# Optimization experiments

Hardware: AMD Instinct MI355X
Metric: run time of the kernel (lower is better)

Reference implementation:

```python
import jax, jax.numpy as jnp
import numpy as np

WS = 7          # window size
NH = 12         # attention heads
D_STATE = 64    # mamba d_state
HEADDIM = 64    # mamba headdim


def layernorm(x, w, b):
    mu = jnp.mean(x, axis=-1, keepdims=True)
    var = jnp.mean((x - mu) ** 2, axis=-1, keepdims=True)
    return (x - mu) * jax.lax.rsqrt(var + 1e-5) * w + b


def mamba2(x, W_in, conv_w, conv_b, dt_bias, A_log, D, mnorm_w, W_out):
    # Mamba2 (SSD) forward: in_proj -> causal depthwise conv+silu -> selective scan -> gated RMSNorm -> out_proj
    B, L, dm = x.shape
    nheads = dt_bias.shape[0]
    d_inner = nheads * HEADDIM
    zxbcdt = x @ W_in                                   # (B,L,2*d_inner+2*d_state+nheads)
    z = zxbcdt[..., :d_inner]
    xBC = zxbcdt[..., d_inner:2 * d_inner + 2 * D_STATE]
    dt = zxbcdt[..., -nheads:]
    conv_dim = xBC.shape[-1]
    pad = conv_w.shape[-1] - 1
    xBC_t = jnp.swapaxes(xBC, 1, 2)                     # (B, conv_dim, L)
    conv_out = jax.lax.conv_general_dilated(
        xBC_t, conv_w[:, None, :], window_strides=(1,), padding=[(pad, 0)],
        feature_group_count=conv_dim, dimension_numbers=('NCH', 'OIH', 'NCH'))
    xBC = jax.nn.silu(jnp.swapaxes(conv_out, 1, 2) + conv_b)
    xs = xBC[..., :d_inner]
    Bm = xBC[..., d_inner:d_inner + D_STATE]            # (B,L,n)
    Cm = xBC[..., d_inner + D_STATE:]                   # (B,L,n)
    dt = jax.nn.softplus(dt + dt_bias)                  # (B,L,h)
    A = -jnp.exp(A_log)                                 # (h,)
    dA = jnp.exp(dt * A)                                # (B,L,h)
    xh = xs.reshape(B, L, nheads, HEADDIM)              # (B,L,h,p)

    def step(h, inp):
        dA_t, dt_t, x_t, B_t, C_t = inp                 # (B,h),(B,h),(B,h,p),(B,n),(B,n)
        dBx = (dt_t[..., None] * x_t)[..., None] * B_t[:, None, None, :]
        h = h * dA_t[..., None, None] + dBx             # (B,h,p,n)
        y = jnp.einsum('bhpn,bn->bhp', h, C_t)
        return h, y

    sw = lambda a: jnp.swapaxes(a, 0, 1)                # time-major
    h0 = jnp.zeros((B, nheads, HEADDIM, D_STATE), x.dtype)
    _, ys = jax.lax.scan(step, h0, (sw(dA), sw(dt), sw(xh), sw(Bm), sw(Cm)))
    y = jnp.swapaxes(ys, 0, 1) + D[None, None, :, None] * xh   # (B,L,h,p)
    y = y.reshape(B, L, d_inner)
    g = y * jax.nn.silu(z)                              # gated RMSNorm (norm_before_gate=False)
    g = g * jax.lax.rsqrt(jnp.mean(g * g, axis=-1, keepdims=True) + 1e-5) * mnorm_w
    return g @ W_out


def gated_window_attention(xw, qkv_w, qkv_b, gate_w, gate_b, proj_w, proj_b):
    B_, N, C = xw.shape
    hd = C // NH
    qkv = (xw @ qkv_w + qkv_b).reshape(B_, N, 3, NH, hd).transpose(2, 0, 3, 1, 4)
    q, k, v = qkv[0] * (hd ** -0.5), qkv[1], qkv[2]     # (B_,h,N,d)
    attn = jax.nn.softmax(jnp.einsum('bhnd,bhmd->bhnm', q, k), axis=-1)
    xa = jnp.einsum('bhnm,bhmd->bhnd', attn, v).transpose(0, 2, 1, 3)  # (B_,N,h,d)
    gate = jax.nn.sigmoid(xw @ gate_w + gate_b)[..., None]             # (B_,N,h,1)
    xa = (xa * gate).reshape(B_, N, C)
    return xa @ proj_w + proj_b


def lgs_forward(x, norm1_w, norm1_b, W_in, conv_w, conv_b, dt_bias, A_log, D, mnorm_w, W_out,
                qkv_w, qkv_b, gate_w, gate_b, proj_w, proj_b, fusion_w, fusion_b,
                norm2_w, norm2_b, fc1_w, fc1_b, fc2_w, fc2_b, H, W):
    B, L, C = x.shape
    shortcut = x
    xn = layernorm(x, norm1_w, norm1_b)
    # Branch A: Mamba2 global scan
    x_mamba = mamba2(xn, W_in, conv_w, conv_b, dt_bias, A_log, D, mnorm_w, W_out)
    # Branch B: gated window attention (shift_size=0 -> no roll, no mask)
    x2d = xn.reshape(B, H, W, C)
    xw = x2d.reshape(B, H // WS, WS, W // WS, WS, C).transpose(0, 1, 3, 2, 4, 5).reshape(-1, WS * WS, C)
    aw = gated_window_attention(xw, qkv_w, qkv_b, gate_w, gate_b, proj_w, proj_b)
    x_attn = aw.reshape(B, H // WS, W // WS, WS, WS, C).transpose(0, 1, 3, 2, 4, 5).reshape(B, L, C)
    # Fuse branches with 1x1 conv (== linear on channel dim)
    x_cat = jnp.concatenate([x_mamba, x_attn], axis=-1)   # (B,L,2C)
    x_fused = x_cat @ fusion_w + fusion_b
    x = shortcut + x_fused
    xn2 = layernorm(x, norm2_w, norm2_b)
    mlp = jax.nn.gelu(xn2 @ fc1_w + fc1_b, approximate=False) @ fc2_w + fc2_b
    return x + mlp


def setup_inputs() -> dict:
    key = jax.random.key(0)
    ks = jax.random.split(key, 16)
    B, H, W, C = 8, 56, 56, 384
    L = H * W
    d_inner, d_state, nheads_m, d_conv = 768, 64, 12, 4
    d_in_proj = 2 * d_inner + 2 * d_state + nheads_m   # 1676
    conv_dim = d_inner + 2 * d_state                   # 896
    s = 0.02
    return {
        'x': jax.random.normal(ks[0], (B, L, C), jnp.float32),
        'norm1_w': jnp.ones((C,), jnp.float32),
        'norm1_b': jnp.zeros((C,), jnp.float32),
        'W_in': jax.random.normal(ks[1], (C, d_in_proj), jnp.float32) * s,
        'conv_w': jax.random.normal(ks[2], (conv_dim, d_conv), jnp.float32) * 0.1,
        'conv_b': jnp.zeros((conv_dim,), jnp.float32),
        'dt_bias': jax.random.normal(ks[3], (nheads_m,), jnp.float32) * 0.5,
        'A_log': jnp.log(jax.random.uniform(ks[4], (nheads_m,), jnp.float32, 1.0, 16.0)),
        'D': jnp.ones((nheads_m,), jnp.float32),
        'mnorm_w': jnp.ones((d_inner,), jnp.float32),
        'W_out': jax.random.normal(ks[5], (d_inner, C), jnp.float32) * s,
        'qkv_w': jax.random.normal(ks[6], (C, 3 * C), jnp.float32) * s,
        'qkv_b': jnp.zeros((3 * C,), jnp.float32),
        'gate_w': jax.random.normal(ks[7], (C, NH), jnp.float32) * s,
        'gate_b': jnp.zeros((NH,), jnp.float32),
        'proj_w': jax.random.normal(ks[8], (C, C), jnp.float32) * s,
        'proj_b': jnp.zeros((C,), jnp.float32),
        'fusion_w': jax.random.normal(ks[9], (2 * C, C), jnp.float32) * s,
        'fusion_b': jnp.zeros((C,), jnp.float32),
        'norm2_w': jnp.ones((C,), jnp.float32),
        'norm2_b': jnp.zeros((C,), jnp.float32),
        'fc1_w': jax.random.normal(ks[10], (C, 4 * C), jnp.float32) * s,
        'fc1_b': jnp.zeros((4 * C,), jnp.float32),
        'fc2_w': jax.random.normal(ks[11], (4 * C, C), jnp.float32) * s,
        'fc2_b': jnp.zeros((C,), jnp.float32),
        'H': H,
        'W': W,
    }


def reference(x, norm1_w, norm1_b, W_in, conv_w, conv_b, dt_bias, A_log, D, mnorm_w, W_out,
              qkv_w, qkv_b, gate_w, gate_b, proj_w, proj_b, fusion_w, fusion_b,
              norm2_w, norm2_b, fc1_w, fc1_b, fc2_w, fc2_b, H, W):
    return lgs_forward(x, norm1_w, norm1_b, W_in, conv_w, conv_b, dt_bias, A_log, D, mnorm_w, W_out,
                       qkv_w, qkv_b, gate_w, gate_b, proj_w, proj_b, fusion_w, fusion_b,
                       norm2_w, norm2_b, fc1_w, fc1_b, fc2_w, fc2_b, H, W)
```

## Files before the change

### kernel.cpp

```cpp
#include <hip/hip_runtime.h>
#include <math.h>

static constexpr int L_SEQ  = 3136;
static constexpr int NBATCH = 8;
static constexpr int CDIM   = 384;
static constexpr int DIN    = 768;
static constexpr int NHM    = 12;
static constexpr int HDM    = 64;
static constexpr int DPROJ  = 1676;
static constexpr int CONVD  = 896;
static constexpr int NROWS  = NBATCH * L_SEQ;
static constexpr int NHA    = 12;
static constexpr int NCH    = 49;
static constexpr int CHT    = 64;
static constexpr int CTK    = 28;

typedef __attribute__((ext_vector_type(8))) short short8;
typedef __attribute__((ext_vector_type(8))) unsigned short ushort8;
typedef __attribute__((ext_vector_type(4))) float f32x4;
typedef const unsigned int __attribute__((address_space(1)))* gua_t;
typedef unsigned int __attribute__((address_space(3)))* lua_t;

__device__ __forceinline__ float siluf(float x) { return x / (1.f + __expf(-x)); }
__device__ __forceinline__ unsigned short f2bf(float f) {
  unsigned int u = __float_as_uint(f);
  u += 0x7fff + ((u >> 16) & 1);
  return (unsigned short)(u >> 16);
}
__device__ __forceinline__ float bf2f(unsigned short h) {
  return __uint_as_float(((unsigned int)h) << 16);
}

__global__ __launch_bounds__(256) void ln_kernel(const float* __restrict__ in,
    const float* __restrict__ w, const float* __restrict__ b, unsigned short* __restrict__ out) {
  int wave = threadIdx.x >> 6, lane = threadIdx.x & 63;
  int row = blockIdx.x * 4 + wave;
  if (row >= NROWS) return;
  const float* r = in + (size_t)row * CDIM;
  float2 v[3];
  float s1 = 0.f, s2 = 0.f;
#pragma unroll
  for (int q = 0; q < 3; q++) {
    v[q] = *(const float2*)&r[q * 128 + lane * 2];
    s1 += v[q].x + v[q].y;
    s2 += v[q].x * v[q].x + v[q].y * v[q].y;
  }
#pragma unroll
  for (int o = 32; o > 0; o >>= 1) { s1 += __shfl_xor(s1, o, 64); s2 += __shfl_xor(s2, o, 64); }
  float mu = s1 * (1.f / 384.f);
  float var = s2 * (1.f / 384.f) - mu * mu;
  float rs = rsqrtf(var + 1e-5f);
  unsigned short* o = out + (size_t)row * CDIM;
#pragma unroll
  for (int q = 0; q < 3; q++) {
    int c = q * 128 + lane * 2;
    float2 wv = *(const float2*)&w[c];
    float2 bv = *(const float2*)&b[c];
    float ox = (v[q].x - mu) * rs * wv.x + bv.x;
    float oy = (v[q].y - mu) * rs * wv.y + bv.y;
    unsigned int pk = (unsigned int)f2bf(ox) | ((unsigned int)f2bf(oy) << 16);
    *(unsigned int*)&o[c] = pk;
  }
}

__global__ __launch_bounds__(256) void wconv_kernel(const float* __restrict__ W,
    unsigned short* __restrict__ WT, int K, int N, int ldw) {
  __shared__ float tile[32][33];
  int k0 = blockIdx.x * 32, n0 = blockIdx.y * 32;
  int tx = threadIdx.x & 31, ty = threadIdx.x >> 5;
#pragma unroll
  for (int j = 0; j < 4; j++) {
    int k = k0 + ty + j * 8;
    int n = n0 + tx;
    tile[ty + j * 8][tx] = (n < N) ? W[(size_t)k * ldw + n] : 0.f;
  }
  __syncthreads();
#pragma unroll
  for (int j = 0; j < 4; j++) {
    int n = n0 + ty + j * 8;
    int k = k0 + tx;
    WT[(size_t)n * K + k] = f2bf(tile[tx][ty + j * 8]);
  }
}

template<int ACT, bool HASBIAS, bool HASRES, bool OUTBF>
__global__ __launch_bounds__(256) void gemm_bf(
    const unsigned short* __restrict__ A, const unsigned short* __restrict__ WT,
    void* __restrict__ Cp, const float* __restrict__ bias,
    const float* __restrict__ res, int ldr,
    int M, int N, int K, int lda, int ldc, int coff)
{
  __shared__ unsigned short As[128][32];
  __shared__ unsigned short Ws[128][32];
  int t = threadIdx.x;
  int m0 = blockIdx.y * 128, n0 = blockIdx.x * 128;
  int lane = t & 63, w = t >> 6;
  int wr = (w >> 1) * 64, wc = (w & 1) * 64;
  int fl = lane & 15, kq = lane >> 4;
  f32x4 acc[4][4];
#pragma unroll
  for (int i = 0; i < 4; i++)
#pragma unroll
    for (int j = 0; j < 4; j++) acc[i][j] = (f32x4)0.f;

  for (int k0 = 0; k0 < K; k0 += 32) {
#pragma unroll
    for (int j = 0; j < 2; j++) {
      int c = j * 256 + t;
      int row = c >> 2, q = c & 3;
      __builtin_amdgcn_global_load_lds(
          (gua_t)&A[(size_t)(m0 + row) * lda + k0 + q * 8],
          (lua_t)&As[0][0] + (size_t)c * 4, 16, 0, 0);
      __builtin_amdgcn_global_load_lds(
          (gua_t)&WT[(size_t)(n0 + row) * K + k0 + q * 8],
          (lua_t)&Ws[0][0] + (size_t)c * 4, 16, 0, 0);
    }
    __syncthreads();
    short8 af[4], bfr[4];
#pragma unroll
    for (int mi = 0; mi < 4; mi++) af[mi] = *(const short8*)&As[wr + mi * 16 + fl][kq * 8];
#pragma unroll
    for (int ni = 0; ni < 4; ni++) bfr[ni] = *(const short8*)&Ws[wc + ni * 16 + fl][kq * 8];
#pragma unroll
    for (int mi = 0; mi < 4; mi++)
#pragma unroll
      for (int ni = 0; ni < 4; ni++)
        acc[mi][ni] = __builtin_amdgcn_mfma_f32_16x16x32_bf16(af[mi], bfr[ni], acc[mi][ni], 0, 0, 0);
    __syncthreads();
  }
  int rbase = (lane >> 4) * 4, cl = lane & 15;
#pragma unroll
  for (int mi = 0; mi < 4; mi++) {
#pragma unroll
    for (int ni = 0; ni < 4; ni++) {
      int n = n0 + wc + ni * 16 + cl;
      if (n >= N) continue;
#pragma unroll
      for (int r = 0; r < 4; r++) {
        int m = m0 + wr + mi * 16 + rbase + r;
        float v = acc[mi][ni][r];
        if (HASBIAS) v += bias[n];
        if (ACT == 1) v = 0.5f * v * (1.f + erff(v * 0.70710678118654752f));
        if (HASRES) v += res[(size_t)m * ldr + n];
        if (OUTBF) ((unsigned short*)Cp)[(size_t)m * ldc + coff + n] = f2bf(v);
        else       ((float*)Cp)[(size_t)m * ldc + coff + n] = v;
      }
    }
  }
}

__global__ void dtprep_kernel(float* __restrict__ DT, const float* __restrict__ dt_bias,
    const float* __restrict__ A_log, float* __restrict__ DA) {
  int idx = blockIdx.x * blockDim.x + threadIdx.x;
  if (idx >= NROWS * NHM) return;
  int h = idx % NHM;
  float v = DT[idx] + dt_bias[h];
  float sp = (v > 20.f) ? v : log1pf(expf(v));
  DT[idx] = sp;
  DA[idx] = -expf(A_log[h]) * sp;
}

__global__ __launch_bounds__(256) void conv_bf_kernel(const unsigned short* __restrict__ xbc,
    const float* __restrict__ cw, const float* __restrict__ cb, unsigned short* __restrict__ XC) {
  int t = blockIdx.x * 256 + threadIdx.x;
  int c8 = t % 112;
  int rg = t / 112;
  int b = rg / 112, lc = rg % 112;
  int l0 = lc * CTK;
  int c0 = c8 * 8;
  float w0[8], w1[8], w2[8], w3[8], bq[8];
#pragma unroll
  for (int i = 0; i < 8; i++) {
    bq[i] = cb[c0 + i];
    float4 w4 = *(const float4*)&cw[(c0 + i) * 4];
    w0[i] = w4.x; w1[i] = w4.y; w2[i] = w4.z; w3[i] = w4.w;
  }
  const unsigned short* base = xbc + (size_t)b * L_SEQ * CONVD + c0;
  unsigned short* obase = XC + (size_t)b * L_SEQ * CONVD + c0;
  ushort8 h0 = (ushort8)0, h1 = (ushort8)0, h2 = (ushort8)0;
  if (l0 >= 3) {
    h0 = *(const ushort8*)&base[(size_t)(l0 - 3) * CONVD];
    h1 = *(const ushort8*)&base[(size_t)(l0 - 2) * CONVD];
    h2 = *(const ushort8*)&base[(size_t)(l0 - 1) * CONVD];
  }
  for (int i = 0; i < CTK; i++) {
    ushort8 cur = *(const ushort8*)&base[(size_t)(l0 + i) * CONVD];
    ushort8 ov;
#pragma unroll
    for (int q = 0; q < 8; q++) {
      float acc = bq[q] + w0[q] * bf2f(h0[q]) + w1[q] * bf2f(h1[q])
                + w2[q] * bf2f(h2[q]) + w3[q] * bf2f(cur[q]);
      ov[q] = f2bf(siluf(acc));
    }
    *(ushort8*)&obase[(size_t)(l0 + i) * CONVD] = ov;
    h0 = h1; h1 = h2; h2 = cur;
  }
}

__global__ __launch_bounds__(256) void mscan1_kernel(const unsigned short* __restrict__ XC,
    const float* __restrict__ dtp, const float* __restrict__ dta,
    float* __restrict__ H, float* __restrict__ QS) {
  __shared__ unsigned short Xt[64 * 72];
  __shared__ unsigned short Bt[64 * 72];
  __shared__ float lcs[64];
  __shared__ float wss[64];
  int ch = blockIdx.x, bh = blockIdx.y;
  int b = bh / NHM, head = bh - b * NHM;
  int t = threadIdx.x;
  int l0 = ch * CHT;
  const unsigned short* xcb = XC + ((size_t)b * L_SEQ + l0) * CONVD;
  if (t < 64) {
    size_t ro = ((size_t)b * L_SEQ + l0 + t) * NHM + head;
    float s = dta[ro];
#pragma unroll
    for (int o = 1; o < 64; o <<= 1) {
      float u = __shfl_up(s, o, 64);
      if (t >= o) s += u;
    }
    float lc63 = __shfl(s, 63, 64);
    lcs[t] = s;
    wss[t] = dtp[ro] * __expf(lc63 - s);
    if (t == 63) QS[bh * NCH + ch] = __expf(s);
  }
  __syncthreads();
#pragma unroll
  for (int it = 0; it < 16; it++) {
    int e = it * 256 + t;
    int j = e >> 6, cc = e & 63;
    const unsigned short* rowp = xcb + (size_t)j * CONVD;
    Xt[cc * 72 + j] = rowp[head * HDM + cc];
    Bt[cc * 72 + j] = f2bf(bf2f(rowp[768 + cc]) * wss[j]);
  }
  __syncthreads();
  int lane = t & 63, w = t >> 6;
  int wr = (w >> 1) * 32, wc = (w & 1) * 32;
  int fl = lane & 15, kq = lane >> 4;
  f32x4 acc[2][2];
#pragma unroll
  for (int i = 0; i < 2; i++)
#pragma unroll
    for (int j = 0; j < 2; j++) acc[i][j] = (f32x4)0.f;
#pragma unroll
  for (int kk = 0; kk < 2; kk++) {
    short8 af[2], bfr[2];
#pragma unroll
    for (int mi = 0; mi < 2; mi++)
      af[mi] = *(const short8*)&Xt[(wr + mi * 16 + fl) * 72 + kk * 32 + kq * 8];
#pragma unroll
    for (int ni = 0; ni < 2; ni++)
      bfr[ni] = *(const short8*)&Bt[(wc + ni * 16 + fl) * 72 + kk * 32 + kq * 8];
#pragma unroll
    for (int mi = 0; mi < 2; mi++)
#pragma unroll
      for (int ni = 0; ni < 2; ni++)
        acc[mi][ni] = __builtin_amdgcn_mfma_f32_16x16x32_bf16(af[mi], bfr[ni], acc[mi][ni], 0, 0, 0);
  }
  float* Hp = H + ((size_t)bh * NCH + ch) * 4096;
  int rbase = kq * 4, cl = fl;
#pragma unroll
  for (int mi = 0; mi < 2; mi++)
#pragma unroll
    for (int ni = 0; ni < 2; ni++)
#pragma unroll
      for (int r = 0; r < 4; r++)
        Hp[(size_t)(wr + mi * 16 + rbase + r) * 64 + wc + ni * 16 + cl] = acc[mi][ni][r];
}

__global__ __launch_bounds__(64) void scomb_kernel(float* __restrict__ H,
    const float* __restrict__ QS) {
  int bh = blockIdx.x;
  int e = (blockIdx.y * 64 + threadIdx.x) * 4;
  float4 cur = make_float4(0.f, 0.f, 0.f, 0.f);
  for (int s = 0; s < NCH; s++) {
    float* Hp = H + ((size_t)bh * NCH + s) * 4096 + e;
    float q = QS[bh * NCH + s];
    float4 tmp = *(float4*)Hp;
    *(float4*)Hp = cur;
    cur.x = q * cur.x + tmp.x;
    cur.y = q * cur.y + tmp.y;
    cur.z = q * cur.z + tmp.z;
    cur.w = q * cur.w + tmp.w;
  }
}

__global__ __launch_bounds__(256) void mscan2_kernel(const unsigned short* __restrict__ XC,
    const float* __restrict__ dtp, const float* __restrict__ dta,
    const float* __restrict__ H, const float* __restrict__ Dp,
    unsigned short* __restrict__ Ybf) {
  __shared__ unsigned short Cs[64 * 72];
  __shared__ unsigned short Bs[64 * 72];
  __shared__ unsigned short Xt[64 * 72];
  __shared__ unsigned short Hs[64 * 72];
  __shared__ unsigned short Ss[64 * 72];
  __shared__ float lcs[64];
  __shared__ float dts[64];
  int ch = blockIdx.x, bh = blockIdx.y;
  int b = bh / NHM, head = bh - b * NHM;
  int t = threadIdx.x;
  int l0 = ch * CHT;
  const unsigned short* xcb = XC + ((size_t)b * L_SEQ + l0) * CONVD;
  const float* Hg = H + ((size_t)bh * NCH + ch) * 4096;
  if (t < 64) {
    size_t ro = ((size_t)b * L_SEQ + l0 + t) * NHM + head;
    float s = dta[ro];
#pragma unroll
    for (int o = 1; o < 64; o <<= 1) {
      float u = __shfl_up(s, o, 64);
      if (t >= o) s += u;
    }
    lcs[t] = s;
    dts[t] = dtp[ro];
  }
#pragma unroll
  for (int it = 0; it < 16; it++) {
    int e = it * 256 + t;
    int j = e >> 6, cc = e & 63;
    const unsigned short* rowp = xcb + (size_t)j * CONVD;
    Xt[cc * 72 + j] = rowp[head * HDM + cc];
    Bs[j * 72 + cc] = rowp[768 + cc];
    Cs[j * 72 + cc] = rowp[832 + cc];
    Hs[j * 72 + cc] = f2bf(Hg[e]);
  }
  __syncthreads();
  int lane = t & 63, w = t >> 6;
  int wr = (w >> 1) * 32, wc = (w & 1) * 32;
  int fl = lane & 15, kq = lane >> 4;
  int rbase = kq * 4, cl = fl;
  f32x4 sacc[2][2];
#pragma unroll
  for (int i = 0; i < 2; i++)
#pragma unroll
    for (int j = 0; j < 2; j++) sacc[i][j] = (f32x4)0.f;
#pragma unroll
  for (int kk = 0; kk < 2; kk++) {
    short8 af[2], bfr[2];
#pragma unroll
    for (int mi = 0; mi < 2; mi++)
      af[mi] = *(const short8*)&Cs[(wr + mi * 16 + fl) * 72 + kk * 32 + kq * 8];
#pragma unroll
    for (int ni = 0; ni < 2; ni++)
      bfr[ni] = *(const short8*)&Bs[(wc + ni * 16 + fl) * 72 + kk * 32 + kq * 8];
#pragma unroll
    for (int mi = 0; mi < 2; mi++)
#pragma unroll
      for (int ni = 0; ni < 2; ni++)
        sacc[mi][ni] = __builtin_amdgcn_mfma_f32_16x16x32_bf16(af[mi], bfr[ni], sacc[mi][ni], 0, 0, 0);
  }
  __syncthreads();
#pragma unroll
  for (int mi = 0; mi < 2; mi++)
#pragma unroll
    for (int ni = 0; ni < 2; ni++)
#pragma unroll
      for (int r = 0; r < 4; r++) {
        int i = wr + mi * 16 + rbase + r;
        int j = wc + ni * 16 + cl;
        float v = (j <= i) ? sacc[mi][ni][r] * dts[j] * __expf(lcs[i] - lcs[j]) : 0.f;
        Ss[i * 72 + j] = f2bf(v);
      }
#pragma unroll
  for (int it = 0; it < 16; it++) {
    int e = it * 256 + t;
    int i = e >> 6, n = e & 63;
    float cv = bf2f(Cs[i * 72 + n]) * __expf(lcs[i]);
    Cs[i * 72 + n] = f2bf(cv);
  }
  __syncthreads();
  f32x4 yacc[2][2];
#pragma unroll
  for (int i = 0; i < 2; i++)
#pragma unroll
    for (int j = 0; j < 2; j++) yacc[i][j] = (f32x4)0.f;
#pragma unroll
  for (int kk = 0; kk < 2; kk++) {
    short8 af[2], bfr[2];
#pragma unroll
    for (int mi = 0; mi < 2; mi++)
      af[mi] = *(const short8*)&Ss[(wr + mi * 16 + fl) * 72 + kk * 32 + kq * 8];
#pragma unroll
    for (int ni = 0; ni < 2; ni++)
      bfr[ni] = *(const short8*)&Xt[(wc + ni * 16 + fl) * 72 + kk * 32 + kq * 8];
#pragma unroll
    for (int mi = 0; mi < 2; mi++)
#pragma unroll
      for (int ni = 0; ni < 2; ni++)
        yacc[mi][ni] = __builtin_amdgcn_mfma_f32_16x16x32_bf16(af[mi], bfr[ni], yacc[mi][ni], 0, 0, 0);
  }
#pragma unroll
  for (int kk = 0; kk < 2; kk++) {
    short8 af[2], bfr[2];
#pragma unroll
    for (int mi = 0; mi < 2; mi++)
      af[mi] = *(const short8*)&Cs[(wr + mi * 16 + fl) * 72 + kk * 32 + kq * 8];
#pragma unroll
    for (int ni = 0; ni < 2; ni++)
      bfr[ni] = *(const short8*)&Hs[(wc + ni * 16 + fl) * 72 + kk * 32 + kq * 8];
#pragma unroll
    for (int mi = 0; mi < 2; mi++)
#pragma unroll
      for (int ni = 0; ni < 2; ni++)
        yacc[mi][ni] = __builtin_amdgcn_mfma_f32_16x16x32_bf16(af[mi], bfr[ni], yacc[mi][ni], 0, 0, 0);
  }
  float Dh = Dp[head];
  unsigned short* yb = Ybf + ((size_t)b * L_SEQ + l0) * DIN + head * HDM;
#pragma unroll
  for (int mi = 0; mi < 2; mi++)
#pragma unroll
    for (int ni = 0; ni < 2; ni++)
#pragma unroll
      for (int r = 0; r < 4; r++) {
        int i = wr + mi * 16 + rbase + r;
        int p = wc + ni * 16 + cl;
        float xval = bf2f(Xt[p * 72 + i]);
        yb[(size_t)i * DIN + p] = f2bf(yacc[mi][ni][r] + Dh * xval);
      }
}

__global__ __launch_bounds__(256) void gate_rms_kernel(unsigned short* __restrict__ Y,
    const unsigned short* __restrict__ Z, const float* __restrict__ mw) {
  int wave = threadIdx.x >> 6, lane = threadIdx.x & 63;
  int row = blockIdx.x * 4 + wave;
  if (row >= NROWS) return;
  unsigned short* y = Y + (size_t)row * DIN;
  const unsigned short* z = Z + (size_t)row * DIN;
  float g[12];
  float ss = 0.f;
#pragma unroll
  for (int q = 0; q < 3; q++) {
    int c = q * 256 + lane * 4;
    uint2 yu = *(const uint2*)&y[c];
    uint2 zu = *(const uint2*)&z[c];
    float y0 = bf2f((unsigned short)(yu.x & 0xffff));
    float y1 = bf2f((unsigned short)(yu.x >> 16));
    float y2 = bf2f((unsigned short)(yu.y & 0xffff));
    float y3 = bf2f((unsigned short)(yu.y >> 16));
    float z0 = bf2f((unsigned short)(zu.x & 0xffff));
    float z1 = bf2f((unsigned short)(zu.x >> 16));
    float z2 = bf2f((unsigned short)(zu.y & 0xffff));
    float z3 = bf2f((unsigned short)(zu.y >> 16));
    float g0 = y0 * siluf(z0), g1 = y1 * siluf(z1);
    float g2 = y2 * siluf(z2), g3 = y3 * siluf(z3);
    ss += g0 * g0 + g1 * g1 + g2 * g2 + g3 * g3;
    g[q * 4 + 0] = g0; g[q * 4 + 1] = g1; g[q * 4 + 2] = g2; g[q * 4 + 3] = g3;
  }
#pragma unroll
  for (int o = 32; o > 0; o >>= 1) ss += __shfl_xor(ss, o, 64);
  float rs = rsqrtf(ss * (1.f / 768.f) + 1e-5f);
#pragma unroll
  for (int q = 0; q < 3; q++) {
    int c = q * 256 + lane * 4;
    float4 m = *(const float4*)&mw[c];
    unsigned int lo = (unsigned int)f2bf(g[q*4+0] * rs * m.x) | ((unsigned int)f2bf(g[q*4+1] * rs * m.y) << 16);
    unsigned int hi = (unsigned int)f2bf(g[q*4+2] * rs * m.z) | ((unsigned int)f2bf(g[q*4+3] * rs * m.w) << 16);
    uint2 pk; pk.x = lo; pk.y = hi;
    *(uint2*)&y[c] = pk;
  }
}

__global__ __launch_bounds__(256) void attgate_kernel(const unsigned short* __restrict__ XN,
    const float* __restrict__ gw, const float* __restrict__ gb, float* __restrict__ G) {
  int wave = threadIdx.x >> 6, lane = threadIdx.x & 63;
  int row = blockIdx.x * 4 + wave;
  if (row >= NROWS) return;
  const unsigned short* x = XN + (size_t)row * CDIM;
  float acc[12] = {};
#pragma unroll
  for (int q = 0; q < 6; q++) {
    int k = q * 64 + lane;
    float xv = bf2f(x[k]);
    const float* wr = gw + (size_t)k * 12;
    float4 w0 = *(const float4*)&wr[0];
    float4 w1 = *(const float4*)&wr[4];
    float4 w2 = *(const float4*)&wr[8];
    acc[0] += xv * w0.x; acc[1] += xv * w0.y; acc[2]  += xv * w0.z; acc[3]  += xv * w0.w;
    acc[4] += xv * w1.x; acc[5] += xv * w1.y; acc[6]  += xv * w1.z; acc[7]  += xv * w1.w;
    acc[8] += xv * w2.x; acc[9] += xv * w2.y; acc[10] += xv * w2.z; acc[11] += xv * w2.w;
  }
#pragma unroll
  for (int h = 0; h < 12; h++)
#pragma unroll
    for (int o = 32; o > 0; o >>= 1) acc[h] += __shfl_xor(acc[h], o, 64);
  if (lane == 0) {
#pragma unroll
    for (int h = 0; h < 12; h++) {
      float v = acc[h] + gb[h];
      G[(size_t)row * 12 + h] = 1.f / (1.f + expf(-v));
    }
  }
}

__global__ __launch_bounds__(256) void attn_kernel(const unsigned short* __restrict__ QKV,
    const float* __restrict__ G, unsigned short* __restrict__ XA) {
  __shared__ float qs[49 * 33];
  __shared__ float kst[32 * 52];
  __shared__ float vs[49 * 32];
  __shared__ float ps[49 * 52];
  int blk = blockIdx.x;
  int head = blk % NHA;
  int win = blk / NHA;
  int b = win >> 6;
  int wr = win & 63;
  int wy = wr >> 3, wx = wr & 7;
  int t = threadIdx.x;
  const float scale = 0.17677669529663688f;

  for (int e = t; e < 1568; e += 256) {
    int tok = e >> 5, d = e & 31;
    int iy = tok / 7, ix = tok - iy * 7;
    size_t rl = (size_t)b * L_SEQ + (wy * 7 + iy) * 56 + (wx * 7 + ix);
    const unsigned short* qp = QKV + rl * 1152 + head * 32 + d;
    qs[tok * 33 + d] = bf2f(qp[0]) * scale;
    kst[d * 52 + tok] = bf2f(qp[384]);
    vs[tok * 32 + d] = bf2f(qp[768]);
  }
  if (t < 96) kst[(t & 31) * 52 + 49 + (t >> 5)] = 0.f;
  __syncthreads();

  for (int e = t; e < 637; e += 256) {
    int qi = e / 13, g = e - qi * 13;
    const float* qrow = &qs[qi * 33];
    float4 acc = make_float4(0.f, 0.f, 0.f, 0.f);
#pragma unroll
    for (int dd = 0; dd < 32; dd++) {
      float qv = qrow[dd];
      float4 kv = *(const float4*)&kst[dd * 52 + g * 4];
      acc.x += qv * kv.x; acc.y += qv * kv.y;
      acc.z += qv * kv.z; acc.w += qv * kv.w;
    }
    *(float4*)&ps[qi * 52 + g * 4] = acc;
  }
  __syncthreads();
  if (t < 49) {
    float* pr = &ps[t * 52];
    float m = pr[0];
    for (int j = 1; j < 49; j++) m = fmaxf(m, pr[j]);
    float s = 0.f;
    for (int j = 0; j < 49; j++) { float e2 = expf(pr[j] - m); pr[j] = e2; s += e2; }
    float inv = 1.f / s;
    for (int j = 0; j < 49; j++) pr[j] *= inv;
  }
  __syncthreads();
  for (int e = t; e < 1568; e += 256) {
    int qi = e >> 5, d = e & 31;
    const float* pr = &ps[qi * 52];
    float acc = 0.f;
    for (int j = 0; j < 49; j++) acc += pr[j] * vs[j * 32 + d];
    int iy = qi / 7, ix = qi - iy * 7;
    size_t rg = (size_t)b * L_SEQ + (wy * 7 + iy) * 56 + (wx * 7 + ix);
    float g = G[rg * 12 + head];
    XA[rg * CDIM + head * 32 + d] = f2bf(acc * g);
  }
}

extern "C" void kernel_launch(void* const* d_in, const int* in_sizes, int n_in,
                              void* d_out, int out_size, void* d_ws, size_t ws_size,
                              hipStream_t stream) {
  const float* x        = (const float*)d_in[0];
  const float* norm1_w  = (const float*)d_in[1];
  const float* norm1_b  = (const float*)d_in[2];
  const float* W_in     = (const float*)d_in[3];
  const float* conv_w   = (const float*)d_in[4];
  const float* conv_b   = (const float*)d_in[5];
  const float* dt_bias  = (const float*)d_in[6];
  const float* A_log    = (const float*)d_in[7];
  const float* Dp       = (const float*)d_in[8];
  const float* mnorm_w  = (const float*)d_in[9];
  const float* W_out    = (const float*)d_in[10];
  const float* qkv_w    = (const float*)d_in[11];
  const float* qkv_b    = (const float*)d_in[12];
  const float* gate_w   = (const float*)d_in[13];
  const float* gate_b   = (const float*)d_in[14];
  const float* proj_w   = (const float*)d_in[15];
  const float* proj_b   = (const float*)d_in[16];
  const float* fusion_w = (const float*)d_in[17];
  const float* fusion_b = (const float*)d_in[18];
  const float* norm2_w  = (const float*)d_in[19];
  const float* norm2_b  = (const float*)d_in[20];
  const float* fc1_w    = (const float*)d_in[21];
  const float* fc1_b    = (const float*)d_in[22];
  const float* fc2_w    = (const float*)d_in[23];
  const float* fc2_b    = (const float*)d_in[24];
  float* OUT = (float*)d_out;

  float* ws = (float*)d_ws;
  unsigned short* XNBF = (unsigned short*)ws;
  float* XC_  = ws + 4816896;
  float* SCR  = XC_ + 22478848;
  unsigned short* YBF = (unsigned short*)(SCR + 22478848);
  unsigned short* WT  = (unsigned short*)(SCR + 22478848 + 9633792);
  float* DT_ = (float*)(WT + 3047424);
  float* DA_ = DT_ + 301056;
  float* G_  = DA_ + 301056;
  float* QS_ = G_  + 301056;

  unsigned short* XBCBF = (unsigned short*)SCR;
  unsigned short* XCBF  = (unsigned short*)XC_;
  float* H_ = SCR;
  unsigned short* ZBF   = (unsigned short*)SCR;
  unsigned short* QKVBF = (unsigned short*)SCR;
  unsigned short* M1BF  = (unsigned short*)SCR;
  unsigned short* CATBF = (unsigned short*)XC_;
  unsigned short* XABF  = (unsigned short*)(XC_ + 9633792);

  unsigned short* wt_xbc  = WT;
  unsigned short* wt_dt   = WT + 344064;
  unsigned short* wt_z    = WT + 393216;
  unsigned short* wt_out  = WT + 688128;
  unsigned short* wt_qkv  = WT + 983040;
  unsigned short* wt_proj = WT + 1425408;
  unsigned short* wt_fus  = WT + 1572864;
  unsigned short* wt_fc1  = WT + 1867776;
  unsigned short* wt_fc2  = WT + 2457600;

  wconv_kernel<<<dim3(12,  28), 256, 0, stream>>>(W_in + 768,  wt_xbc,  384,  896, DPROJ);
  wconv_kernel<<<dim3(12,   4), 256, 0, stream>>>(W_in + 1664, wt_dt,   384,   12, DPROJ);
  wconv_kernel<<<dim3(12,  24), 256, 0, stream>>>(W_in,        wt_z,    384,  768, DPROJ);
  wconv_kernel<<<dim3(24,  12), 256, 0, stream>>>(W_out,       wt_out,  768,  384, 384);
  wconv_kernel<<<dim3(12,  36), 256, 0, stream>>>(qkv_w,       wt_qkv,  384, 1152, 1152);
  wconv_kernel<<<dim3(12,  12), 256, 0, stream>>>(proj_w,      wt_proj, 384,  384, 384);
  wconv_kernel<<<dim3(24,  12), 256, 0, stream>>>(fusion_w,    wt_fus,  768,  384, 384);
  wconv_kernel<<<dim3(12,  48), 256, 0, stream>>>(fc1_w,       wt_fc1,  384, 1536, 1536);
  wconv_kernel<<<dim3(48,  12), 256, 0, stream>>>(fc2_w,       wt_fc2, 1536,  384, 384);

  ln_kernel<<<6272, 256, 0, stream>>>(x, norm1_w, norm1_b, XNBF);

  gemm_bf<0, false, false, true><<<dim3(7, 196), 256, 0, stream>>>(
      XNBF, wt_xbc, XBCBF, nullptr, nullptr, 0, NROWS, CONVD, CDIM, CDIM, CONVD, 0);
  conv_bf_kernel<<<392, 256, 0, stream>>>(XBCBF, conv_w, conv_b, XCBF);
  gemm_bf<0, false, false, false><<<dim3(1, 196), 256, 0, stream>>>(
      XNBF, wt_dt, DT_, nullptr, nullptr, 0, NROWS, NHM, CDIM, CDIM, NHM, 0);

  dtprep_kernel<<<(NROWS * NHM + 255) / 256, 256, 0, stream>>>(DT_, dt_bias, A_log, DA_);

  mscan1_kernel<<<dim3(NCH, 96), 256, 0, stream>>>(XCBF, DT_, DA_, H_, QS_);
  scomb_kernel<<<dim3(96, 16), 64, 0, stream>>>(H_, QS_);
  mscan2_kernel<<<dim3(NCH, 96), 256, 0, stream>>>(XCBF, DT_, DA_, H_, Dp, YBF);

  gemm_bf<0, false, false, true><<<dim3(6, 196), 256, 0, stream>>>(
      XNBF, wt_z, ZBF, nullptr, nullptr, 0, NROWS, DIN, CDIM, CDIM, DIN, 0);
  gate_rms_kernel<<<6272, 256, 0, stream>>>(YBF, ZBF, mnorm_w);

  gemm_bf<0, false, false, true><<<dim3(3, 196), 256, 0, stream>>>(
      YBF, wt_out, CATBF, nullptr, nullptr, 0, NROWS, CDIM, DIN, DIN, 2 * CDIM, 0);

  attgate_kernel<<<6272, 256, 0, stream>>>(XNBF, gate_w, gate_b, G_);

  gemm_bf<0, true, false, true><<<dim3(9, 196), 256, 0, stream>>>(
      XNBF, wt_qkv, QKVBF, qkv_b, nullptr, 0, NROWS, 3 * CDIM, CDIM, CDIM, 3 * CDIM, 0);
  attn_kernel<<<512 * NHA, 256, 0, stream>>>(QKVBF, G_, XABF);

  gemm_bf<0, true, false, true><<<dim3(3, 196), 256, 0, stream>>>(
      XABF, wt_proj, CATBF, proj_b, nullptr, 0, NROWS, CDIM, CDIM, CDIM, 2 * CDIM, CDIM);

  gemm_bf<0, true, true, false><<<dim3(3, 196), 256, 0, stream>>>(
      CATBF, wt_fus, OUT, fusion_b, x, CDIM, NROWS, CDIM, 2 * CDIM, 2 * CDIM, CDIM, 0);

  ln_kernel<<<6272, 256, 0, stream>>>(OUT, norm2_w, norm2_b, XNBF);

  gemm_bf<1, true, false, true><<<dim3(12, 196), 256, 0, stream>>>(
      XNBF, wt_fc1, M1BF, fc1_b, nullptr, 0, NROWS, 4 * CDIM, CDIM, CDIM, 4 * CDIM, 0);
  gemm_bf<0, true, true, false><<<dim3(3, 196), 256, 0, stream>>>(
      M1BF, wt_fc2, OUT, fc2_b, OUT, CDIM, NROWS, CDIM, 4 * CDIM, 4 * CDIM, CDIM, 0);
}
```

Before: 798.0 us.

## Triple-buffer GEMM LDS loads, swizzle LDS, remap workgroups per XCD, fast erf

The bf16 MFMA GEMM now keeps three LDS buffers and issues the next k-tile's global-to-LDS loads before computing on the current one. It waits with vmcnt and a single barrier per iteration instead of two syncthreads. LDS columns are XOR-swizzled to reduce bank conflicts, and workgroup IDs are remapped so consecutive tiles land on the same XCD for L2 locality. The GELU epilogue uses an Abramowitz–Stegun erf approximation instead of erff, which trades some accuracy for cheaper math.

```diff
diff --git a/kernel.cpp b/kernel.cpp
--- a/kernel.cpp
+++ b/kernel.cpp
@@ -30,6 +30,14 @@
 __device__ __forceinline__ float bf2f(unsigned short h) {
   return __uint_as_float(((unsigned int)h) << 16);
 }
+__device__ __forceinline__ float fast_erff(float x) {
+  float ax = fabsf(x);
+  float tt = 1.f / (1.f + 0.3275911f * ax);
+  float y = tt * (0.254829592f + tt * (-0.284496736f + tt * (1.421413741f +
+            tt * (-1.453152027f + tt * 1.061405429f))));
+  float r = 1.f - y * __expf(-ax * ax);
+  return copysignf(r, x);
+}
 
 __global__ __launch_bounds__(256) void ln_kernel(const float* __restrict__ in,
     const float* __restrict__ w, const float* __restrict__ b, unsigned short* __restrict__ out) {
@@ -90,43 +98,67 @@
     const float* __restrict__ res, int ldr,
     int M, int N, int K, int lda, int ldc, int coff)
 {
-  __shared__ unsigned short As[128][32];
-  __shared__ unsigned short Ws[128][32];
+  __shared__ unsigned short As[3][128][32];
+  __shared__ unsigned short Ws[3][128][32];
   int t = threadIdx.x;
-  int m0 = blockIdx.y * 128, n0 = blockIdx.x * 128;
+  int gx = gridDim.x;
+  int nwg = gx * gridDim.y;
+  int orig = blockIdx.y * gx + blockIdx.x;
+  int qq = nwg >> 3, rr = nwg & 7;
+  int xcd = orig & 7, seq = orig >> 3;
+  int wgid = (xcd < rr ? xcd * (qq + 1) : rr * (qq + 1) + (xcd - rr) * qq) + seq;
+  int m0 = (wgid / gx) * 128, n0 = (wgid % gx) * 128;
+
   int lane = t & 63, w = t >> 6;
   int wr = (w >> 1) * 64, wc = (w & 1) * 64;
   int fl = lane & 15, kq = lane >> 4;
+  int so = ((kq ^ ((lane >> 1) & 3))) * 8;
   f32x4 acc[4][4];
 #pragma unroll
   for (int i = 0; i < 4; i++)
 #pragma unroll
     for (int j = 0; j < 4; j++) acc[i][j] = (f32x4)0.f;
 
-  for (int k0 = 0; k0 < K; k0 += 32) {
+  auto stage = [&](int buf, int k0) {
 #pragma unroll
     for (int j = 0; j < 2; j++) {
       int c = j * 256 + t;
-      int row = c >> 2, q = c & 3;
+      int row = c >> 2, qs = c & 3;
+      int qsrc = qs ^ ((row >> 1) & 3);
       __builtin_amdgcn_global_load_lds(
-          (gua_t)&A[(size_t)(m0 + row) * lda + k0 + q * 8],
-          (lua_t)&As[0][0] + (size_t)c * 4, 16, 0, 0);
+          (gua_t)&A[(size_t)(m0 + row) * lda + k0 + qsrc * 8],
+          (lua_t)&As[buf][0][0] + (size_t)c * 4, 16, 0, 0);
       __builtin_amdgcn_global_load_lds(
-          (gua_t)&WT[(size_t)(n0 + row) * K + k0 + q * 8],
-          (lua_t)&Ws[0][0] + (size_t)c * 4, 16, 0, 0);
-    }
-    __syncthreads();
+          (gua_t)&WT[(size_t)(n0 + row) * K + k0 + qsrc * 8],
+          (lua_t)&Ws[buf][0][0] + (size_t)c * 4, 16, 0, 0);
+    }
+  };
+
+  int nk = K >> 5;
+  stage(0, 0);
+  int sb = 1, rb = 0;
+  for (int ks = 0; ks < nk; ks++) {
+    if (ks + 1 < nk) {
+      stage(sb, (ks + 1) << 5);
+      sb = sb == 2 ? 0 : sb + 1;
+      asm volatile("s_waitcnt vmcnt(4)" ::: "memory");
+    } else {
+      asm volatile("s_waitcnt vmcnt(0)" ::: "memory");
+    }
+    __builtin_amdgcn_s_barrier();
+    asm volatile("" ::: "memory");
+    __builtin_amdgcn_sched_barrier(0);
     short8 af[4], bfr[4];
 #pragma unroll
-    for (int mi = 0; mi < 4; mi++) af[mi] = *(const short8*)&As[wr + mi * 16 + fl][kq * 8];
-#pragma unroll
-    for (int ni = 0; ni < 4; ni++) bfr[ni] = *(const short8*)&Ws[wc + ni * 16 + fl][kq * 8];
+    for (int mi = 0; mi < 4; mi++) af[mi] = *(const short8*)&As[rb][wr + mi * 16 + fl][so];
+#pragma unroll
+    for (int ni = 0; ni < 4; ni++) bfr[ni] = *(const short8*)&Ws[rb][wc + ni * 16 + fl][so];
+    rb = rb == 2 ? 0 : rb + 1;
 #pragma unroll
     for (int mi = 0; mi < 4; mi++)
 #pragma unroll
       for (int ni = 0; ni < 4; ni++)
         acc[mi][ni] = __builtin_amdgcn_mfma_f32_16x16x32_bf16(af[mi], bfr[ni], acc[mi][ni], 0, 0, 0);
-    __syncthreads();
   }
   int rbase = (lane >> 4) * 4, cl = lane & 15;
 #pragma unroll
@@ -140,7 +172,7 @@
         int m = m0 + wr + mi * 16 + rbase + r;
         float v = acc[mi][ni][r];
         if (HASBIAS) v += bias[n];
-        if (ACT == 1) v = 0.5f * v * (1.f + erff(v * 0.70710678118654752f));
+        if (ACT == 1) v = 0.5f * v * (1.f + fast_erff(v * 0.70710678118654752f));
         if (HASRES) v += res[(size_t)m * ldr + n];
         if (OUTBF) ((unsigned short*)Cp)[(size_t)m * ldc + coff + n] = f2bf(v);
         else       ((float*)Cp)[(size_t)m * ldc + coff + n] = v;
```

New measurement: 742.1 us. 7.0% less time.
